# Kernel tuning notes

Measured on AMD Instinct MI355X. Metric: run time of the kernel, lower is better.

Reference implementation:

```python
import jax, jax.numpy as jnp
import numpy as np

D_MODEL = 1024
N_HEAD = 16
D_K = D_MODEL // N_HEAD
B, S = 2, 2048


def setup_inputs() -> dict:
    key = jax.random.key(0)
    ks = jax.random.split(key, 13)
    sc = 0.02
    return {
        "q": jax.random.normal(ks[0], (B, S, D_MODEL), jnp.float32),
        "k": jax.random.normal(ks[1], (B, S, D_MODEL), jnp.float32),
        "v": jax.random.normal(ks[2], (B, S, D_MODEL), jnp.float32),
        "mask": jax.random.randint(ks[3], (B, 1, S, S), 0, 2, jnp.int32),
        "Wq": jax.random.normal(ks[4], (D_MODEL, D_MODEL), jnp.float32) * sc,
        "bq": jnp.zeros((D_MODEL,), jnp.float32),
        "Wk": jax.random.normal(ks[5], (D_MODEL, D_MODEL), jnp.float32) * sc,
        "bk": jnp.zeros((D_MODEL,), jnp.float32),
        "Wv": jax.random.normal(ks[6], (D_MODEL, D_MODEL), jnp.float32) * sc,
        "bv": jnp.zeros((D_MODEL,), jnp.float32),
        "Wo": jax.random.normal(ks[7], (D_MODEL, D_MODEL), jnp.float32) * sc,
        "bo": jnp.zeros((D_MODEL,), jnp.float32),
    }


def _split_head(x):
    # (B, S, D) -> (B, H, S, d_k)
    b, s, _ = x.shape
    return x.reshape(b, s, N_HEAD, D_K).transpose(0, 2, 1, 3)


def reference(q, k, v, mask, Wq, bq, Wk, bk, Wv, bv, Wo, bo):
    qh = _split_head(q @ Wq.T + bq)
    kh = _split_head(k @ Wk.T + bk)
    vh = _split_head(v @ Wv.T + bv)
    # NOTE: original scales by sqrt(d_model), not sqrt(d_k)
    score = jnp.einsum("bhqd,bhkd->bhqk", qh, kh) / jnp.sqrt(jnp.float32(D_MODEL))
    score = jnp.where(mask == 0, jnp.float32(-1e9), score)
    attn = jax.nn.softmax(score, axis=-1)
    out = jnp.einsum("bhqk,bhkd->bhqd", attn, vh)
    out = out.transpose(0, 2, 1, 3).reshape(q.shape[0], -1, D_MODEL)
    return out @ Wo.T + bo
```

## Files before the change

kernel.cpp:

```cpp
#include <hip/hip_runtime.h>

#define D_MODEL 1024
#define N_HEAD  16
#define D_K     64
#define BATCH   2
#define SEQ     2048
#define M_ROWS  (BATCH*SEQ)
#define NT      (SEQ/64)

typedef __attribute__((ext_vector_type(8))) short short8;
typedef __attribute__((ext_vector_type(4))) float f32x4;
typedef unsigned short u16;
typedef unsigned long long u64;

#define GLDS16(g, l) \
    __builtin_amdgcn_global_load_lds((const __attribute__((address_space(1))) void*)(g), \
                                     (__attribute__((address_space(3))) void*)(l), 16, 0, 0)

__device__ __forceinline__ u16 f2bf(float f) {
    unsigned u = __builtin_bit_cast(unsigned, f);
    unsigned r = (u + 0x7fffu + ((u >> 16) & 1u)) >> 16;
    return (u16)r;
}

__device__ __forceinline__ float fexp2(float x) {
#if __has_builtin(__builtin_amdgcn_exp2f)
    return __builtin_amdgcn_exp2f(x);
#else
    return exp2f(x);
#endif
}

template<int CTRL>
__device__ __forceinline__ float dppmov(float x) {
    return __builtin_bit_cast(float,
        __builtin_amdgcn_mov_dpp(__builtin_bit_cast(int, x), CTRL, 0xf, 0xf, true));
}
__device__ __forceinline__ float rowmax16(float x) {
    x = fmaxf(x, dppmov<0xB1>(x));
    x = fmaxf(x, dppmov<0x4E>(x));
    x = fmaxf(x, dppmov<0x124>(x));
    x = fmaxf(x, dppmov<0x128>(x));
    return x;
}
__device__ __forceinline__ float rowsum16(float x) {
    x += dppmov<0xB1>(x);
    x += dppmov<0x4E>(x);
    x += dppmov<0x124>(x);
    x += dppmov<0x128>(x);
    return x;
}

__global__ __launch_bounds__(256)
void cvt_all(const float* __restrict__ q, const float* __restrict__ k, const float* __restrict__ v,
             const float* __restrict__ wq, const float* __restrict__ wk,
             const float* __restrict__ wv, const float* __restrict__ wo,
             u16* __restrict__ qb, u16* __restrict__ kb, u16* __restrict__ vb,
             u16* __restrict__ wqb, u16* __restrict__ wkb, u16* __restrict__ wvb, u16* __restrict__ wob)
{
    const int total = 3 * 1048576 + 4 * 262144;
    int i = blockIdx.x * blockDim.x + threadIdx.x;
    const int stride = gridDim.x * blockDim.x;
    for (; i < total; i += stride) {
        const float* src; u16* dst; int loc;
        if (i < 3 * 1048576) {
            const int t = i >> 20; loc = i & 1048575;
            src = (t == 0) ? q : (t == 1) ? k : v;
            dst = (t == 0) ? qb : (t == 1) ? kb : vb;
        } else {
            const int j = i - 3 * 1048576; const int t = j >> 18; loc = j & 262143;
            src = (t == 0) ? wq : (t == 1) ? wk : (t == 2) ? wv : wo;
            dst = (t == 0) ? wqb : (t == 1) ? wkb : (t == 2) ? wvb : wob;
        }
        float4 a = ((const float4*)src)[loc];
        ushort4 o;
        o.x = f2bf(a.x); o.y = f2bf(a.y); o.z = f2bf(a.z); o.w = f2bf(a.w);
        ((ushort4*)dst)[loc] = o;
    }
}

__global__ __launch_bounds__(256)
void mask_pack(const int* __restrict__ mask, u64* __restrict__ mb, int nwords)
{
    const int lane = threadIdx.x & 63;
    int w = (blockIdx.x * blockDim.x + threadIdx.x) >> 6;
    const int nw = (gridDim.x * blockDim.x) >> 6;
    for (; w < nwords; w += nw) {
        int v = mask[(size_t)w * 64 + lane];
        u64 bits = __ballot(v != 0);
        if (lane == 0) mb[w] = bits;
    }
}

template<bool OUT_BF16, bool BIAS_ROW>
__device__ __forceinline__
void gemm_body(const u16* __restrict__ A, const u16* __restrict__ W,
               const float* __restrict__ bias, void* __restrict__ Cout,
               const int M, const int N, const int K, const int bx, const int by)
{
    __shared__ u16 As[2][128 * 32];
    __shared__ u16 Ws[2][64 * 32];
    const int tid = threadIdx.x, l = tid & 63, w = tid >> 6;
    const int bm = by * 128, bn = bx * 64;
    const int wr = (w >> 1) * 64, wc = (w & 1) * 32;

    const int srow = tid >> 2, scol = (tid & 3) * 8;
    const u16* Ap = A + (size_t)(bm + srow) * K + scol;
    const u16* Wp = W + (size_t)(bn + srow) * K + scol;

    f32x4 acc[4][2];
#pragma unroll
    for (int m = 0; m < 4; ++m)
#pragma unroll
        for (int n = 0; n < 2; ++n) acc[m][n] = (f32x4)0.0f;

    const int ro = l & 15, ge = (l >> 4) * 8;

    GLDS16(Ap,                  (char*)As[0] + w * 1024);
    GLDS16(Ap + (size_t)64 * K, (char*)As[0] + w * 1024 + 4096);
    GLDS16(Wp,                  (char*)Ws[0] + w * 1024);
    __syncthreads();

    int buf = 0;
    for (int k0 = 0; k0 < K; k0 += 32) {
        if (k0 + 32 < K) {
            GLDS16(Ap + k0 + 32,                  (char*)As[buf ^ 1] + w * 1024);
            GLDS16(Ap + k0 + 32 + (size_t)64 * K, (char*)As[buf ^ 1] + w * 1024 + 4096);
            GLDS16(Wp + k0 + 32,                  (char*)Ws[buf ^ 1] + w * 1024);
        }
        short8 a[4], b[2];
#pragma unroll
        for (int m = 0; m < 4; ++m)
            a[m] = *(const short8*)(As[buf] + (wr + m * 16 + ro) * 32 + ge);
#pragma unroll
        for (int n = 0; n < 2; ++n)
            b[n] = *(const short8*)(Ws[buf] + (wc + n * 16 + ro) * 32 + ge);
#pragma unroll
        for (int m = 0; m < 4; ++m)
#pragma unroll
            for (int n = 0; n < 2; ++n)
                acc[m][n] = __builtin_amdgcn_mfma_f32_16x16x32_bf16(a[m], b[n], acc[m][n], 0, 0, 0);
        __syncthreads();
        buf ^= 1;
    }

    const int cr = (l >> 4) * 4;
#pragma unroll
    for (int m = 0; m < 4; ++m)
#pragma unroll
        for (int n = 0; n < 2; ++n)
#pragma unroll
            for (int j = 0; j < 4; ++j) {
                const int row = bm + wr + m * 16 + cr + j;
                const int col = bn + wc + n * 16 + ro;
                const float vvv = acc[m][n][j] + (BIAS_ROW ? bias[row] : bias[col]);
                if constexpr (OUT_BF16)
                    ((u16*)Cout)[(size_t)row * N + col] = f2bf(vvv);
                else
                    ((float*)Cout)[(size_t)row * N + col] = vvv;
            }
}

__device__ __forceinline__ void xcd_swizzle(int gx, int gy, int& bx, int& by)
{
    int lin = blockIdx.y * gx + blockIdx.x;
    const int nwg = gx * gy;
    const int cpx = nwg >> 3;
    lin = (lin & 7) * cpx + (lin >> 3);
    bx = lin % gx; by = lin / gx;
}

__global__ __launch_bounds__(256)
void gemm_qk(const u16* __restrict__ qb, const u16* __restrict__ kb,
             const u16* __restrict__ wqb, const u16* __restrict__ wkb,
             const float* __restrict__ bq, const float* __restrict__ bk,
             u16* __restrict__ Qp, u16* __restrict__ Kp)
{
    int bx, by; xcd_swizzle(gridDim.x, gridDim.y, bx, by);
    const int z = blockIdx.z;
    gemm_body<true, false>(z ? kb : qb, z ? wkb : wqb, z ? bk : bq,
                           z ? Kp : Qp, M_ROWS, D_MODEL, D_MODEL, bx, by);
}

__global__ __launch_bounds__(256)
void gemm_vt(const u16* __restrict__ wvb, const u16* __restrict__ vb,
             const float* __restrict__ bv, u16* __restrict__ Vt)
{
    int bx, by; xcd_swizzle(gridDim.x, gridDim.y, bx, by);
    gemm_body<true, true>(wvb, vb, bv, Vt, D_MODEL, M_ROWS, D_MODEL, bx, by);
}

__global__ __launch_bounds__(256)
void gemm_out(const u16* __restrict__ Ctx, const u16* __restrict__ wob,
              const float* __restrict__ bo, float* __restrict__ out)
{
    int bx, by; xcd_swizzle(gridDim.x, gridDim.y, bx, by);
    gemm_body<false, false>(Ctx, wob, bo, out, M_ROWS, D_MODEL, D_MODEL, bx, by);
}

__global__ __launch_bounds__(256, 4)
void attn_mfma(const u16* __restrict__ Qp, const u16* __restrict__ Kp,
               const u16* __restrict__ Vt, const u64* __restrict__ mb,
               u16* __restrict__ Ctx)
{
    __shared__ char QsPs[8192];
    __shared__ char Ks[2][8192];
    __shared__ char Vs[2][8192];

    const int tid = threadIdx.x, l = tid & 63, w = tid >> 6;
    int lin = blockIdx.y * gridDim.x + blockIdx.x;
    lin = (lin & 7) * 128 + (lin >> 3);
    const int bx = lin & 31, by = lin >> 5;
    const int b = by >> 4, h = by & 15;
    const int q0 = bx * 64;
    const size_t tokbase = (size_t)b * SEQ;

    const int lrow = tid >> 3, ss = (tid & 7) ^ (lrow & 7);
    const u16* ksrc0 = Kp + (tokbase + lrow) * D_MODEL + h * 64 + ss * 8;
    const u16* vsrc0 = Vt + (size_t)(h * 64 + lrow) * M_ROWS + tokbase + ss * 8;

    {
        const u16* qsrc = Qp + (tokbase + q0 + lrow) * D_MODEL + h * 64 + ss * 8;
        GLDS16(qsrc,                          QsPs + w * 1024);
        GLDS16(qsrc + (size_t)32 * D_MODEL,   QsPs + w * 1024 + 4096);
        GLDS16(ksrc0,                         (char*)Ks[0] + w * 1024);
        GLDS16(ksrc0 + (size_t)32 * D_MODEL,  (char*)Ks[0] + w * 1024 + 4096);
        GLDS16(vsrc0,                         (char*)Vs[0] + w * 1024);
        GLDS16(vsrc0 + (size_t)32 * M_ROWS,   (char*)Vs[0] + w * 1024 + 4096);
    }
    __syncthreads();

    const int ro = l & 15, gb = (l >> 4) * 16;

    short8 qf[2];
#pragma unroll
    for (int c = 0; c < 2; ++c) {
        const int row = w * 16 + ro;
        qf[c] = *(const short8*)(QsPs + row * 128 + ((c * 64 + gb) ^ ((row & 7) << 4)));
    }

    size_t mbase[4];
#pragma unroll
    for (int j = 0; j < 4; ++j)
        mbase[j] = (tokbase + q0 + w * 16 + (l >> 4) * 4 + j) * (size_t)NT;

    f32x4 o[4];
    float m_s[4], l_s[4];
#pragma unroll
    for (int j = 0; j < 4; ++j) { m_s[j] = -1e30f; l_s[j] = 0.f; }
#pragma unroll
    for (int dn = 0; dn < 4; ++dn) o[dn] = (f32x4)0.0f;

    constexpr float CSC = 0.03125f * 1.44269504089f;

    for (int t = 0; t < NT; ++t) {
        const int cur = t & 1;
        if (t + 1 < NT) {
            const u16* kn = ksrc0 + (size_t)(t + 1) * 64 * D_MODEL;
            const u16* vn = vsrc0 + (t + 1) * 64;
            GLDS16(kn,                         (char*)Ks[cur ^ 1] + w * 1024);
            GLDS16(kn + (size_t)32 * D_MODEL,  (char*)Ks[cur ^ 1] + w * 1024 + 4096);
            GLDS16(vn,                         (char*)Vs[cur ^ 1] + w * 1024);
            GLDS16(vn + (size_t)32 * M_ROWS,   (char*)Vs[cur ^ 1] + w * 1024 + 4096);
        }

        u64 mw[4];
#pragma unroll
        for (int j = 0; j < 4; ++j) mw[j] = mb[mbase[j] + t];

        f32x4 s[4];
#pragma unroll
        for (int n = 0; n < 4; ++n) {
            const int row = n * 16 + ro;
            short8 k0f = *(const short8*)(Ks[cur] + row * 128 + ((gb)      ^ ((row & 7) << 4)));
            short8 k1f = *(const short8*)(Ks[cur] + row * 128 + ((64 + gb) ^ ((row & 7) << 4)));
            f32x4 a = (f32x4)0.0f;
            a = __builtin_amdgcn_mfma_f32_16x16x32_bf16(qf[0], k0f, a, 0, 0, 0);
            a = __builtin_amdgcn_mfma_f32_16x16x32_bf16(qf[1], k1f, a, 0, 0, 0);
            s[n] = a;
        }

        float rmx[4];
        int pred = 1;
#pragma unroll
        for (int j = 0; j < 4; ++j) {
            const u64 t64 = mw[j] >> ro;
#pragma unroll
            for (int n = 0; n < 4; ++n)
                s[n][j] = ((t64 >> (n * 16)) & 1) ? s[n][j] * CSC : -1e9f;
            float rm = fmaxf(fmaxf(s[0][j], s[1][j]), fmaxf(s[2][j], s[3][j]));
            rm = rowmax16(rm);
            rmx[j] = rm;
            pred &= (rm <= m_s[j] + 8.f);
        }
        if (!__all(pred)) {
#pragma unroll
            for (int j = 0; j < 4; ++j) {
                const float mn = fmaxf(m_s[j], rmx[j]);
                const float al = fexp2(m_s[j] - mn);
                m_s[j] = mn; l_s[j] *= al;
                o[0][j] *= al; o[1][j] *= al; o[2][j] *= al; o[3][j] *= al;
            }
        }

        char* pb = QsPs + w * 2048;
#pragma unroll
        for (int j = 0; j < 4; ++j) {
            const int prow = (l >> 4) * 4 + j;
            const int sw = (prow & 7) << 4;
            const float p0 = fexp2(s[0][j] - m_s[j]);
            const float p1 = fexp2(s[1][j] - m_s[j]);
            const float p2 = fexp2(s[2][j] - m_s[j]);
            const float p3 = fexp2(s[3][j] - m_s[j]);
            float rs = (p0 + p1) + (p2 + p3);
            rs = rowsum16(rs);
            l_s[j] += rs;
            *(u16*)(pb + prow * 128 + ((2 * (0  + ro)) ^ sw)) = f2bf(p0);
            *(u16*)(pb + prow * 128 + ((2 * (16 + ro)) ^ sw)) = f2bf(p1);
            *(u16*)(pb + prow * 128 + ((2 * (32 + ro)) ^ sw)) = f2bf(p2);
            *(u16*)(pb + prow * 128 + ((2 * (48 + ro)) ^ sw)) = f2bf(p3);
        }

        short8 pf[2];
#pragma unroll
        for (int c = 0; c < 2; ++c)
            pf[c] = *(const short8*)(pb + ro * 128 + ((c * 64 + gb) ^ ((ro & 7) << 4)));
#pragma unroll
        for (int dn = 0; dn < 4; ++dn) {
            const int row = dn * 16 + ro;
            short8 v0f = *(const short8*)(Vs[cur] + row * 128 + ((gb)      ^ ((row & 7) << 4)));
            short8 v1f = *(const short8*)(Vs[cur] + row * 128 + ((64 + gb) ^ ((row & 7) << 4)));
            o[dn] = __builtin_amdgcn_mfma_f32_16x16x32_bf16(pf[0], v0f, o[dn], 0, 0, 0);
            o[dn] = __builtin_amdgcn_mfma_f32_16x16x32_bf16(pf[1], v1f, o[dn], 0, 0, 0);
        }

        __syncthreads();
    }

    float inv[4];
#pragma unroll
    for (int j = 0; j < 4; ++j) inv[j] = 1.f / l_s[j];
#pragma unroll
    for (int dn = 0; dn < 4; ++dn)
#pragma unroll
        for (int j = 0; j < 4; ++j) {
            const size_t qr = tokbase + q0 + w * 16 + (l >> 4) * 4 + j;
            Ctx[qr * D_MODEL + h * 64 + dn * 16 + ro] = f2bf(o[dn][j] * inv[j]);
        }
}

extern "C" void kernel_launch(void* const* d_in, const int* in_sizes, int n_in,
                              void* d_out, int out_size, void* d_ws, size_t ws_size,
                              hipStream_t stream)
{
    const float* q    = (const float*)d_in[0];
    const float* k    = (const float*)d_in[1];
    const float* v    = (const float*)d_in[2];
    const int*   mask = (const int*)  d_in[3];
    const float* Wq   = (const float*)d_in[4];
    const float* bq   = (const float*)d_in[5];
    const float* Wk   = (const float*)d_in[6];
    const float* bk   = (const float*)d_in[7];
    const float* Wv   = (const float*)d_in[8];
    const float* bv   = (const float*)d_in[9];
    const float* Wo   = (const float*)d_in[10];
    const float* bo   = (const float*)d_in[11];
    float* out = (float*)d_out;

    u16* ws16 = (u16*)d_ws;
    const size_t M1 = 1024 * 1024;
    u16* qb  = ws16;
    u16* kb  = ws16 + 4 * M1;
    u16* vb  = ws16 + 8 * M1;
    u16* Wqb = ws16 + 12 * M1;
    u16* Wkb = ws16 + 13 * M1;
    u16* Wvb = ws16 + 14 * M1;
    u16* Wob = ws16 + 15 * M1;
    u16* Qp  = ws16 + 16 * M1;
    u16* Kp  = ws16 + 20 * M1;
    u16* Vt  = ws16 + 24 * M1;
    u16* Ctx = qb;
    u64* maskb = (u64*)vb;

    cvt_all<<<2048, 256, 0, stream>>>(q, k, v, Wq, Wk, Wv, Wo,
                                      qb, kb, vb, Wqb, Wkb, Wvb, Wob);

    dim3 gqk(D_MODEL / 64, M_ROWS / 128, 2);
    gemm_qk<<<gqk, 256, 0, stream>>>(qb, kb, Wqb, Wkb, bq, bk, Qp, Kp);

    dim3 gvt(M_ROWS / 64, D_MODEL / 128);
    gemm_vt<<<gvt, 256, 0, stream>>>(Wvb, vb, bv, Vt);

    mask_pack<<<1024, 256, 0, stream>>>(mask, maskb, BATCH * SEQ * SEQ / 64);

    dim3 ga(SEQ / 64, BATCH * N_HEAD);
    attn_mfma<<<ga, 256, 0, stream>>>(Qp, Kp, Vt, maskb, Ctx);

    dim3 go(D_MODEL / 64, M_ROWS / 128);
    gemm_out<<<go, 256, 0, stream>>>(Ctx, Wob, bo, out);
}
```

Baseline: 325.1 us.

## Drop online softmax max tracking, fold scale into Q, merge projection GEMMs

```diff
diff --git a/kernel.cpp b/kernel.cpp
--- a/kernel.cpp
+++ b/kernel.cpp
@@ -17,6 +17,8 @@
     __builtin_amdgcn_global_load_lds((const __attribute__((address_space(1))) void*)(g), \
                                      (__attribute__((address_space(3))) void*)(l), 16, 0, 0)
 
+#define CSC (0.03125f * 1.44269504089f)
+
 __device__ __forceinline__ u16 f2bf(float f) {
     unsigned u = __builtin_bit_cast(unsigned, f);
     unsigned r = (u + 0x7fffu + ((u >> 16) & 1u)) >> 16;
@@ -29,26 +31,6 @@
 #else
     return exp2f(x);
 #endif
-}
-
-template<int CTRL>
-__device__ __forceinline__ float dppmov(float x) {
-    return __builtin_bit_cast(float,
-        __builtin_amdgcn_mov_dpp(__builtin_bit_cast(int, x), CTRL, 0xf, 0xf, true));
-}
-__device__ __forceinline__ float rowmax16(float x) {
-    x = fmaxf(x, dppmov<0xB1>(x));
-    x = fmaxf(x, dppmov<0x4E>(x));
-    x = fmaxf(x, dppmov<0x124>(x));
-    x = fmaxf(x, dppmov<0x128>(x));
-    return x;
-}
-__device__ __forceinline__ float rowsum16(float x) {
-    x += dppmov<0xB1>(x);
-    x += dppmov<0x4E>(x);
-    x += dppmov<0x124>(x);
-    x += dppmov<0x128>(x);
-    return x;
 }
 
 __global__ __launch_bounds__(256)
@@ -92,33 +74,33 @@
     }
 }
 
-template<bool OUT_BF16, bool BIAS_ROW>
+template<bool OUT_BF16, bool BIAS_ROW, bool SCALE>
 __device__ __forceinline__
-void gemm_body(const u16* __restrict__ A, const u16* __restrict__ W,
-               const float* __restrict__ bias, void* __restrict__ Cout,
-               const int M, const int N, const int K, const int bx, const int by)
+void gemm128_body(const u16* __restrict__ A, const u16* __restrict__ W,
+                  const float* __restrict__ bias, void* __restrict__ Cout,
+                  const int M, const int N, const int K, const int bx, const int by)
 {
     __shared__ u16 As[2][128 * 32];
-    __shared__ u16 Ws[2][64 * 32];
+    __shared__ u16 Ws[2][128 * 32];
     const int tid = threadIdx.x, l = tid & 63, w = tid >> 6;
-    const int bm = by * 128, bn = bx * 64;
-    const int wr = (w >> 1) * 64, wc = (w & 1) * 32;
-
+    const int bm = by * 128, bn = bx * 128;
+    const int wr = (w >> 1) * 64, wc = (w & 1) * 64;
     const int srow = tid >> 2, scol = (tid & 3) * 8;
     const u16* Ap = A + (size_t)(bm + srow) * K + scol;
     const u16* Wp = W + (size_t)(bn + srow) * K + scol;
 
-    f32x4 acc[4][2];
+    f32x4 acc[4][4];
 #pragma unroll
     for (int m = 0; m < 4; ++m)
 #pragma unroll
-        for (int n = 0; n < 2; ++n) acc[m][n] = (f32x4)0.0f;
+        for (int n = 0; n < 4; ++n) acc[m][n] = (f32x4)0.0f;
 
     const int ro = l & 15, ge = (l >> 4) * 8;
 
     GLDS16(Ap,                  (char*)As[0] + w * 1024);
     GLDS16(Ap + (size_t)64 * K, (char*)As[0] + w * 1024 + 4096);
     GLDS16(Wp,                  (char*)Ws[0] + w * 1024);
+    GLDS16(Wp + (size_t)64 * K, (char*)Ws[0] + w * 1024 + 4096);
     __syncthreads();
 
     int buf = 0;
@@ -127,18 +109,19 @@
             GLDS16(Ap + k0 + 32,                  (char*)As[buf ^ 1] + w * 1024);
             GLDS16(Ap + k0 + 32 + (size_t)64 * K, (char*)As[buf ^ 1] + w * 1024 + 4096);
             GLDS16(Wp + k0 + 32,                  (char*)Ws[buf ^ 1] + w * 1024);
-        }
-        short8 a[4], b[2];
+            GLDS16(Wp + k0 + 32 + (size_t)64 * K, (char*)Ws[buf ^ 1] + w * 1024 + 4096);
+        }
+        short8 a[4], b[4];
 #pragma unroll
         for (int m = 0; m < 4; ++m)
             a[m] = *(const short8*)(As[buf] + (wr + m * 16 + ro) * 32 + ge);
 #pragma unroll
-        for (int n = 0; n < 2; ++n)
+        for (int n = 0; n < 4; ++n)
             b[n] = *(const short8*)(Ws[buf] + (wc + n * 16 + ro) * 32 + ge);
 #pragma unroll
         for (int m = 0; m < 4; ++m)
 #pragma unroll
-            for (int n = 0; n < 2; ++n)
+            for (int n = 0; n < 4; ++n)
                 acc[m][n] = __builtin_amdgcn_mfma_f32_16x16x32_bf16(a[m], b[n], acc[m][n], 0, 0, 0);
         __syncthreads();
         buf ^= 1;
@@ -148,12 +131,13 @@
 #pragma unroll
     for (int m = 0; m < 4; ++m)
 #pragma unroll
-        for (int n = 0; n < 2; ++n)
+        for (int n = 0; n < 4; ++n)
 #pragma unroll
             for (int j = 0; j < 4; ++j) {
                 const int row = bm + wr + m * 16 + cr + j;
                 const int col = bn + wc + n * 16 + ro;
-                const float vvv = acc[m][n][j] + (BIAS_ROW ? bias[row] : bias[col]);
+                float vvv = acc[m][n][j] + (BIAS_ROW ? bias[row] : bias[col]);
+                if constexpr (SCALE) vvv *= CSC;
                 if constexpr (OUT_BF16)
                     ((u16*)Cout)[(size_t)row * N + col] = f2bf(vvv);
                 else
@@ -161,41 +145,95 @@
             }
 }
 
-__device__ __forceinline__ void xcd_swizzle(int gx, int gy, int& bx, int& by)
-{
-    int lin = blockIdx.y * gx + blockIdx.x;
-    const int nwg = gx * gy;
-    const int cpx = nwg >> 3;
-    lin = (lin & 7) * cpx + (lin >> 3);
-    bx = lin % gx; by = lin / gx;
-}
-
 __global__ __launch_bounds__(256)
-void gemm_qk(const u16* __restrict__ qb, const u16* __restrict__ kb,
-             const u16* __restrict__ wqb, const u16* __restrict__ wkb,
-             const float* __restrict__ bq, const float* __restrict__ bk,
-             u16* __restrict__ Qp, u16* __restrict__ Kp)
-{
-    int bx, by; xcd_swizzle(gridDim.x, gridDim.y, bx, by);
-    const int z = blockIdx.z;
-    gemm_body<true, false>(z ? kb : qb, z ? wkb : wqb, z ? bk : bq,
-                           z ? Kp : Qp, M_ROWS, D_MODEL, D_MODEL, bx, by);
-}
-
-__global__ __launch_bounds__(256)
-void gemm_vt(const u16* __restrict__ wvb, const u16* __restrict__ vb,
-             const float* __restrict__ bv, u16* __restrict__ Vt)
-{
-    int bx, by; xcd_swizzle(gridDim.x, gridDim.y, bx, by);
-    gemm_body<true, true>(wvb, vb, bv, Vt, D_MODEL, M_ROWS, D_MODEL, bx, by);
+void gemm_proj(const u16* __restrict__ qb, const u16* __restrict__ kb, const u16* __restrict__ vb,
+               const u16* __restrict__ wqb, const u16* __restrict__ wkb, const u16* __restrict__ wvb,
+               const float* __restrict__ bq, const float* __restrict__ bk, const float* __restrict__ bv,
+               u16* __restrict__ Qp, u16* __restrict__ Kp, u16* __restrict__ Vt)
+{
+    int lin = blockIdx.x;
+    lin = (lin & 7) * 32 + (lin >> 3);
+    const int z = blockIdx.y;
+    if (z == 0)
+        gemm128_body<true, false, true >(qb, wqb, bq, Qp, M_ROWS, D_MODEL, D_MODEL, lin & 7, lin >> 3);
+    else if (z == 1)
+        gemm128_body<true, false, false>(kb, wkb, bk, Kp, M_ROWS, D_MODEL, D_MODEL, lin & 7, lin >> 3);
+    else
+        gemm128_body<true, true,  false>(wvb, vb, bv, Vt, D_MODEL, M_ROWS, D_MODEL, lin & 31, lin >> 5);
+}
+
+__device__ __forceinline__
+void gemm64_body(const u16* __restrict__ A, const u16* __restrict__ W,
+                 const float* __restrict__ bias, float* __restrict__ Cout,
+                 const int N, const int K, const int bx, const int by)
+{
+    __shared__ u16 As[2][128 * 32];
+    __shared__ u16 Ws[2][64 * 32];
+    const int tid = threadIdx.x, l = tid & 63, w = tid >> 6;
+    const int bm = by * 128, bn = bx * 64;
+    const int wr = (w >> 1) * 64, wc = (w & 1) * 32;
+    const int srow = tid >> 2, scol = (tid & 3) * 8;
+    const u16* Ap = A + (size_t)(bm + srow) * K + scol;
+    const u16* Wp = W + (size_t)(bn + srow) * K + scol;
+
+    f32x4 acc[4][2];
+#pragma unroll
+    for (int m = 0; m < 4; ++m)
+#pragma unroll
+        for (int n = 0; n < 2; ++n) acc[m][n] = (f32x4)0.0f;
+
+    const int ro = l & 15, ge = (l >> 4) * 8;
+
+    GLDS16(Ap,                  (char*)As[0] + w * 1024);
+    GLDS16(Ap + (size_t)64 * K, (char*)As[0] + w * 1024 + 4096);
+    GLDS16(Wp,                  (char*)Ws[0] + w * 1024);
+    __syncthreads();
+
+    int buf = 0;
+    for (int k0 = 0; k0 < K; k0 += 32) {
+        if (k0 + 32 < K) {
+            GLDS16(Ap + k0 + 32,                  (char*)As[buf ^ 1] + w * 1024);
+            GLDS16(Ap + k0 + 32 + (size_t)64 * K, (char*)As[buf ^ 1] + w * 1024 + 4096);
+            GLDS16(Wp + k0 + 32,                  (char*)Ws[buf ^ 1] + w * 1024);
+        }
+        short8 a[4], b[2];
+#pragma unroll
+        for (int m = 0; m < 4; ++m)
+            a[m] = *(const short8*)(As[buf] + (wr + m * 16 + ro) * 32 + ge);
+#pragma unroll
+        for (int n = 0; n < 2; ++n)
+            b[n] = *(const short8*)(Ws[buf] + (wc + n * 16 + ro) * 32 + ge);
+#pragma unroll
+        for (int m = 0; m < 4; ++m)
+#pragma unroll
+            for (int n = 0; n < 2; ++n)
+                acc[m][n] = __builtin_amdgcn_mfma_f32_16x16x32_bf16(a[m], b[n], acc[m][n], 0, 0, 0);
+        __syncthreads();
+        buf ^= 1;
+    }
+
+    const int cr = (l >> 4) * 4;
+#pragma unroll
+    for (int m = 0; m < 4; ++m)
+#pragma unroll
+        for (int n = 0; n < 2; ++n)
+#pragma unroll
+            for (int j = 0; j < 4; ++j) {
+                const int row = bm + wr + m * 16 + cr + j;
+                const int col = bn + wc + n * 16 + ro;
+                Cout[(size_t)row * N + col] = acc[m][n][j] + bias[col];
+            }
 }
 
 __global__ __launch_bounds__(256)
 void gemm_out(const u16* __restrict__ Ctx, const u16* __restrict__ wob,
               const float* __restrict__ bo, float* __restrict__ out)
 {
-    int bx, by; xcd_swizzle(gridDim.x, gridDim.y, bx, by);
-    gemm_body<false, false>(Ctx, wob, bo, out, M_ROWS, D_MODEL, D_MODEL, bx, by);
+    int lin = blockIdx.y * gridDim.x + blockIdx.x;
+    const int cpx = (gridDim.x * gridDim.y) >> 3;
+    lin = (lin & 7) * cpx + (lin >> 3);
+    const int bx = lin % gridDim.x, by = lin / gridDim.x;
+    gemm64_body(Ctx, wob, bo, out, D_MODEL, D_MODEL, bx, by);
 }
 
 __global__ __launch_bounds__(256, 4)
@@ -239,22 +277,28 @@
         qf[c] = *(const short8*)(QsPs + row * 128 + ((c * 64 + gb) ^ ((row & 7) << 4)));
     }
 
-    size_t mbase[4];
+    const uint2* mptr[4];
 #pragma unroll
     for (int j = 0; j < 4; ++j)
-        mbase[j] = (tokbase + q0 + w * 16 + (l >> 4) * 4 + j) * (size_t)NT;
-
-    f32x4 o[4];
-    float m_s[4], l_s[4];
-#pragma unroll
-    for (int j = 0; j < 4; ++j) { m_s[j] = -1e30f; l_s[j] = 0.f; }
+        mptr[j] = (const uint2*)(mb + (tokbase + q0 + w * 16 + (l >> 4) * 4 + j) * (size_t)NT);
+
+    f32x4 o[4], lacc = (f32x4)0.0f;
 #pragma unroll
     for (int dn = 0; dn < 4; ++dn) o[dn] = (f32x4)0.0f;
 
-    constexpr float CSC = 0.03125f * 1.44269504089f;
+    const short8 ones = {0x3F80, 0x3F80, 0x3F80, 0x3F80, 0x3F80, 0x3F80, 0x3F80, 0x3F80};
+
+    uint2 mw[4];
+#pragma unroll
+    for (int j = 0; j < 4; ++j) mw[j] = mptr[j][0];
 
     for (int t = 0; t < NT; ++t) {
         const int cur = t & 1;
+
+        uint2 mc[4];
+#pragma unroll
+        for (int j = 0; j < 4; ++j) mc[j] = mw[j];
+
         if (t + 1 < NT) {
             const u16* kn = ksrc0 + (size_t)(t + 1) * 64 * D_MODEL;
             const u16* vn = vsrc0 + (t + 1) * 64;
@@ -262,11 +306,9 @@
             GLDS16(kn + (size_t)32 * D_MODEL,  (char*)Ks[cur ^ 1] + w * 1024 + 4096);
             GLDS16(vn,                         (char*)Vs[cur ^ 1] + w * 1024);
             GLDS16(vn + (size_t)32 * M_ROWS,   (char*)Vs[cur ^ 1] + w * 1024 + 4096);
-        }
-
-        u64 mw[4];
-#pragma unroll
-        for (int j = 0; j < 4; ++j) mw[j] = mb[mbase[j] + t];
+#pragma unroll
+            for (int j = 0; j < 4; ++j) mw[j] = mptr[j][t + 1];
+        }
 
         f32x4 s[4];
 #pragma unroll
@@ -280,51 +322,34 @@
             s[n] = a;
         }
 
-        float rmx[4];
-        int pred = 1;
-#pragma unroll
-        for (int j = 0; j < 4; ++j) {
-            const u64 t64 = mw[j] >> ro;
-#pragma unroll
-            for (int n = 0; n < 4; ++n)
-                s[n][j] = ((t64 >> (n * 16)) & 1) ? s[n][j] * CSC : -1e9f;
-            float rm = fmaxf(fmaxf(s[0][j], s[1][j]), fmaxf(s[2][j], s[3][j]));
-            rm = rowmax16(rm);
-            rmx[j] = rm;
-            pred &= (rm <= m_s[j] + 8.f);
-        }
-        if (!__all(pred)) {
-#pragma unroll
-            for (int j = 0; j < 4; ++j) {
-                const float mn = fmaxf(m_s[j], rmx[j]);
-                const float al = fexp2(m_s[j] - mn);
-                m_s[j] = mn; l_s[j] *= al;
-                o[0][j] *= al; o[1][j] *= al; o[2][j] *= al; o[3][j] *= al;
-            }
-        }
-
         char* pb = QsPs + w * 2048;
 #pragma unroll
         for (int j = 0; j < 4; ++j) {
             const int prow = (l >> 4) * 4 + j;
             const int sw = (prow & 7) << 4;
-            const float p0 = fexp2(s[0][j] - m_s[j]);
-            const float p1 = fexp2(s[1][j] - m_s[j]);
-            const float p2 = fexp2(s[2][j] - m_s[j]);
-            const float p3 = fexp2(s[3][j] - m_s[j]);
-            float rs = (p0 + p1) + (p2 + p3);
-            rs = rowsum16(rs);
-            l_s[j] += rs;
-            *(u16*)(pb + prow * 128 + ((2 * (0  + ro)) ^ sw)) = f2bf(p0);
-            *(u16*)(pb + prow * 128 + ((2 * (16 + ro)) ^ sw)) = f2bf(p1);
-            *(u16*)(pb + prow * 128 + ((2 * (32 + ro)) ^ sw)) = f2bf(p2);
-            *(u16*)(pb + prow * 128 + ((2 * (48 + ro)) ^ sw)) = f2bf(p3);
+            const unsigned wlo = mc[j].x >> ro;
+            const unsigned whi = mc[j].y >> ro;
+            float p0 = fexp2(s[0][j]); p0 = (wlo & 1u)       ? p0 : 0.f;
+            float p1 = fexp2(s[1][j]); p1 = (wlo & 0x10000u) ? p1 : 0.f;
+            float p2 = fexp2(s[2][j]); p2 = (whi & 1u)       ? p2 : 0.f;
+            float p3 = fexp2(s[3][j]); p3 = (whi & 0x10000u) ? p3 : 0.f;
+            unsigned pk01, pk23;
+            asm("v_cvt_pk_bf16_f32 %0, %1, %2" : "=v"(pk01) : "v"(p0), "v"(p1));
+            asm("v_cvt_pk_bf16_f32 %0, %1, %2" : "=v"(pk23) : "v"(p2), "v"(p3));
+            *(u16*)(pb + prow * 128 + ((2 * (0  + ro)) ^ sw)) = (u16)pk01;
+            *(u16*)(pb + prow * 128 + ((2 * (16 + ro)) ^ sw)) = (u16)(pk01 >> 16);
+            *(u16*)(pb + prow * 128 + ((2 * (32 + ro)) ^ sw)) = (u16)pk23;
+            *(u16*)(pb + prow * 128 + ((2 * (48 + ro)) ^ sw)) = (u16)(pk23 >> 16);
         }
 
         short8 pf[2];
 #pragma unroll
         for (int c = 0; c < 2; ++c)
             pf[c] = *(const short8*)(pb + ro * 128 + ((c * 64 + gb) ^ ((ro & 7) << 4)));
+
+        lacc = __builtin_amdgcn_mfma_f32_16x16x32_bf16(pf[0], ones, lacc, 0, 0, 0);
+        lacc = __builtin_amdgcn_mfma_f32_16x16x32_bf16(pf[1], ones, lacc, 0, 0, 0);
+
 #pragma unroll
         for (int dn = 0; dn < 4; ++dn) {
             const int row = dn * 16 + ro;
@@ -339,7 +364,7 @@
 
     float inv[4];
 #pragma unroll
-    for (int j = 0; j < 4; ++j) inv[j] = 1.f / l_s[j];
+    for (int j = 0; j < 4; ++j) inv[j] = 1.f / lacc[j];
 #pragma unroll
     for (int dn = 0; dn < 4; ++dn)
 #pragma unroll
@@ -385,11 +410,8 @@
     cvt_all<<<2048, 256, 0, stream>>>(q, k, v, Wq, Wk, Wv, Wo,
                                       qb, kb, vb, Wqb, Wkb, Wvb, Wob);
 
-    dim3 gqk(D_MODEL / 64, M_ROWS / 128, 2);
-    gemm_qk<<<gqk, 256, 0, stream>>>(qb, kb, Wqb, Wkb, bq, bk, Qp, Kp);
-
-    dim3 gvt(M_ROWS / 64, D_MODEL / 128);
-    gemm_vt<<<gvt, 256, 0, stream>>>(Wvb, vb, bv, Vt);
+    dim3 gproj(256, 3);
+    gemm_proj<<<gproj, 256, 0, stream>>>(qb, kb, vb, Wqb, Wkb, Wvb, bq, bk, bv, Qp, Kp, Vt);
 
     mask_pack<<<1024, 256, 0, stream>>>(mask, maskb, BATCH * SEQ * SEQ / 64);
 
```

Result: faster. 306.1 us (-5.9%).
